# Kernel optimization log

Hardware: AMD Instinct MI355X
Metric: run time of the kernel (lower is better)

## Reference

```python
import jax, jax.numpy as jnp
from jax import lax
import numpy as np

B, C_IN, H, W = 4, 3, 128, 128
K, D = 8192, 16  # num_embeddings, embedding_size (= encoder out channels)


def _conv(x, w, b):
    # x: (B,C,H,W), w: (O,I,3,3) OIHW, VALID padding, stride 1
    y = lax.conv_general_dilated(x, w, (1, 1), 'VALID',
                                 dimension_numbers=('NCHW', 'OIHW', 'NCHW'))
    return y + b[None, :, None, None]


def _conv_t(x, w, b):
    # transpose conv, stride 1, k=3: correlate with flipped/transposed kernel, pad 2
    # w: (I,O,3,3) -> flip spatial, swap to OIHW
    wk = jnp.flip(w, (2, 3)).transpose(1, 0, 2, 3)
    y = lax.conv_general_dilated(x, wk, (1, 1), [(2, 2), (2, 2)],
                                 dimension_numbers=('NCHW', 'OIHW', 'NCHW'))
    return y + b[None, :, None, None]


def setup_inputs() -> dict:
    key = jax.random.key(0)
    ks = jax.random.split(key, 14)
    g = lambda k, shp, fan: jax.random.normal(k, shp, jnp.float32) / np.float32(np.sqrt(fan))
    return {
        'x':   jax.random.normal(ks[0], (B, C_IN, H, W), jnp.float32),
        'ew1': g(ks[1], (4, C_IN, 3, 3), C_IN * 9), 'eb1': jnp.zeros((4,), jnp.float32),
        'ew2': g(ks[2], (8, 4, 3, 3), 4 * 9),       'eb2': jnp.zeros((8,), jnp.float32),
        'ew3': g(ks[3], (16, 8, 3, 3), 8 * 9),      'eb3': jnp.zeros((16,), jnp.float32),
        'dw1': g(ks[4], (16, 8, 3, 3), 16 * 9),     'db1': jnp.zeros((8,), jnp.float32),
        'dw2': g(ks[5], (8, 4, 3, 3), 8 * 9),       'db2': jnp.zeros((4,), jnp.float32),
        'dw3': g(ks[6], (4, C_IN, 3, 3), 4 * 9),    'db3': jnp.zeros((C_IN,), jnp.float32),
        'codebook': jax.random.normal(ks[7], (K, D), jnp.float32) * 0.02,
    }


def reference(x, ew1, eb1, ew2, eb2, ew3, eb3, dw1, db1, dw2, db2, dw3, db3, codebook):
    # encode
    z = jax.nn.selu(_conv(x, ew1, eb1))
    z = jax.nn.selu(_conv(z, ew2, eb2))
    z = _conv(z, ew3, eb3)                      # (B, D, h, w)
    b, d, h, w = z.shape
    zf = z.transpose(0, 2, 3, 1).reshape(-1, d)  # (N, D) flattened latents
    # ||z - e||^2 = ||z||^2 - 2 z.e + ||e||^2, argmin over codebook rows
    d2 = ((zf * zf).sum(1, keepdims=True)
          - 2.0 * (zf @ codebook.T)
          + (codebook * codebook).sum(1)[None, :])  # (N, K)
    idx = jnp.argmin(d2, axis=1)                 # (N,) int32
    zq = codebook[idx].reshape(b, h, w, d).transpose(0, 3, 1, 2)  # gather + reshape
    # decode
    y = jax.nn.selu(_conv_t(zq, dw1, db1))
    y = jax.nn.selu(_conv_t(y, dw2, db2))
    y = _conv_t(y, dw3, db3)                     # (B, C_IN, H, W)
    return (y, idx)
```

## Files before the change

kernel.cpp:

```cpp
#include <hip/hip_runtime.h>
#include <math.h>

#define BATCH 4
#define DLAT 16
#define KCB 8192
#define HLAT 122
#define PIX (HLAT*HLAT)
#define NLAT (BATCH*PIX)
#define NKT (KCB/16)
#define NVQBLK 931
#define KTW (NKT/4)
#define CAPW 1024
#define NCONVBLK 3721

typedef _Float16 half8 __attribute__((ext_vector_type(8)));
typedef float f32x4 __attribute__((ext_vector_type(4)));

__device__ __forceinline__ float selu_np(float x) {
    const float scale = 1.0507009873554805f, alpha = 1.6732632423543772f;
    if (x > 0.f) return __fmul_rn(scale, x);
    return __fmul_rn(scale, __fmul_rn(alpha, expm1f(x)));
}

template<int CI, int CO, int HIN, int WIN, bool DOSELU>
__global__ void conv3x3_np(const float* __restrict__ in, const float* __restrict__ w,
                           const float* __restrict__ bias, float* __restrict__ out) {
    constexpr int HO = HIN - 2, WO = WIN - 2;
    int tid = blockIdx.x * blockDim.x + threadIdx.x;
    constexpr int total = BATCH * CO * HO * WO;
    if (tid >= total) return;
    int j = tid % WO; int t = tid / WO;
    int i = t % HO;   t /= HO;
    int o = t % CO;   int b = t / CO;
    float acc = 0.f;
    for (int c = 0; c < CI; ++c) {
        const float* ip = in + ((b * CI + c) * HIN + i) * WIN + j;
        const float* wp = w + ((o * CI + c) * 3) * 3;
        #pragma unroll
        for (int p = 0; p < 3; ++p)
            #pragma unroll
            for (int q = 0; q < 3; ++q)
                acc = __fmaf_rn(ip[p * WIN + q], wp[p * 3 + q], acc);
    }
    acc = __fadd_rn(acc, bias[o]);
    out[tid] = DOSELU ? selu_np(acc) : acc;
}

__global__ void conv3_last_np(const float* __restrict__ in, const float* __restrict__ w,
                              const float* __restrict__ bias, float* __restrict__ zf,
                              _Float16* __restrict__ zh, float* __restrict__ blockmax) {
    constexpr int CI = 8, HIN = 124, WIN = 124, WO = 122;
    __shared__ float sred[4];
    int tid = blockIdx.x * 256 + threadIdx.x;
    int o  = tid & 15;
    int pp = tid >> 4;
    int b = pp / PIX, pix = pp % PIX;
    int i = pix / WO, j = pix % WO;
    float acc = 0.f;
    for (int c = 0; c < CI; ++c) {
        const float* ip = in + ((b * CI + c) * HIN + i) * WIN + j;
        const float* wp = w + ((o * CI + c) * 3) * 3;
        #pragma unroll
        for (int p = 0; p < 3; ++p)
            #pragma unroll
            for (int q = 0; q < 3; ++q)
                acc = __fmaf_rn(ip[p * WIN + q], wp[p * 3 + q], acc);
    }
    acc = __fadd_rn(acc, bias[o]);
    zf[tid] = acc;
    zh[tid] = (_Float16)acc;
    float m = fabsf(acc);
    #pragma unroll
    for (int off = 32; off; off >>= 1) m = fmaxf(m, __shfl_xor(m, off));
    if ((threadIdx.x & 63) == 0) sred[threadIdx.x >> 6] = m;
    __syncthreads();
    if (threadIdx.x == 0)
        blockmax[blockIdx.x] = fmaxf(fmaxf(sred[0], sred[1]), fmaxf(sred[2], sred[3]));
}

__global__ void reduce_zmax(const float* __restrict__ bm, unsigned* __restrict__ scal) {
    __shared__ float sred[4];
    float m = 0.f;
    for (int i = threadIdx.x; i < NCONVBLK; i += 256) m = fmaxf(m, bm[i]);
    #pragma unroll
    for (int off = 32; off; off >>= 1) m = fmaxf(m, __shfl_xor(m, off));
    if ((threadIdx.x & 63) == 0) sred[threadIdx.x >> 6] = m;
    __syncthreads();
    if (threadIdx.x == 0)
        scal[0] = __float_as_uint(fmaxf(fmaxf(sred[0], sred[1]), fmaxf(sred[2], sred[3])));
}

__device__ __forceinline__ float pairwise16_sq(const float* v) {
    float a[16];
    #pragma unroll
    for (int d = 0; d < 16; ++d) a[d] = __fmul_rn(v[d], v[d]);
    float r0 = __fadd_rn(a[0], a[8]),  r1 = __fadd_rn(a[1], a[9]);
    float r2 = __fadd_rn(a[2], a[10]), r3 = __fadd_rn(a[3], a[11]);
    float r4 = __fadd_rn(a[4], a[12]), r5 = __fadd_rn(a[5], a[13]);
    float r6 = __fadd_rn(a[6], a[14]), r7 = __fadd_rn(a[7], a[15]);
    return __fadd_rn(__fadd_rn(__fadd_rn(r0, r1), __fadd_rn(r2, r3)),
                     __fadd_rn(__fadd_rn(r4, r5), __fadd_rn(r6, r7)));
}

__device__ __forceinline__ void load16(const float* __restrict__ p, float* v) {
    const float4* r = (const float4*)p;
    float4 v0 = r[0], v1 = r[1], v2 = r[2], v3 = r[3];
    v[0]=v0.x; v[1]=v0.y; v[2]=v0.z; v[3]=v0.w;
    v[4]=v1.x; v[5]=v1.y; v[6]=v1.z; v[7]=v1.w;
    v[8]=v2.x; v[9]=v2.y; v[10]=v2.z; v[11]=v2.w;
    v[12]=v3.x; v[13]=v3.y; v[14]=v3.z; v[15]=v3.w;
}

__device__ __forceinline__ float np_d2(const float* zr, float A, const float* e16, float cnk) {
    float g = 0.f;
    #pragma unroll
    for (int d = 0; d < 16; ++d) g = __fmaf_rn(zr[d], e16[d], g);
    return __fadd_rn(__fmaf_rn(-2.f, g, A), cnk);
}

__global__ void init_scal(unsigned* scal) { scal[0] = 0u; scal[1] = 0u; }

__global__ void cbprep(const float* __restrict__ cb, float* __restrict__ cn,
                       _Float16* __restrict__ cbB, unsigned* __restrict__ scal) {
    int k = blockIdx.x * 256 + threadIdx.x;
    float v[16];
    load16(cb + (size_t)k * DLAT, v);
    float C = pairwise16_sq(v);
    cn[k] = C;
    float m = C;
    #pragma unroll
    for (int off = 32; off; off >>= 1) m = fmaxf(m, __shfl_xor(m, off));
    if ((threadIdx.x & 63) == 0) atomicMax(&scal[1], __float_as_uint(m));
    int kt = k >> 4, col = k & 15;
    #pragma unroll
    for (int d = 0; d < 16; ++d) {
        int ln = (d >> 3) * 16 + col;
        cbB[((size_t)(kt * 32 + ln)) * 8 + (d & 7)] = (_Float16)v[d];
    }
}

__global__ __launch_bounds__(256, 4) void vq_mfma(
        const _Float16* __restrict__ zh, const float* __restrict__ zf,
        const _Float16* __restrict__ cbB, const float* __restrict__ cn,
        const float* __restrict__ cb, const unsigned* __restrict__ scal,
        float* __restrict__ idx_out, float* __restrict__ zq) {
    __shared__ unsigned list[CAPW];
    __shared__ float resd[CAPW];
    __shared__ float smin[4][64];
    __shared__ unsigned lcnt;
    const int tid = threadIdx.x;
    const int w = tid >> 6, lane = tid & 63;
    const int R0 = blockIdx.x * 64;
    const half8 hz = {0,0,0,0,0,0,0,0};
    const f32x4 zero4 = {0.f, 0.f, 0.f, 0.f};
    if (tid == 0) lcnt = 0;

    half8 a[4];
    #pragma unroll
    for (int f = 0; f < 4; ++f) {
        int r = R0 + f * 16 + (lane & 15);
        if (r >= NLAT) r = NLAT - 1;
        a[f] = (lane < 32) ? *(const half8*)(zh + (size_t)r * DLAT + (lane >> 4) * 8) : hz;
    }

    float zmaxf = __uint_as_float(scal[0]);
    float en    = sqrtf(__uint_as_float(scal[1]));
    float errG  = 4.f * zmaxf * en * 9.765625e-4f * 1.03f
                + 6.104e-5f * (16.f * zmaxf + 4.f * en);
    float slack = (16.f * zmaxf * zmaxf + 8.f * zmaxf * en + en * en) * 1.2e-7f;
    float DELTA = 4.f * errG + 2.f * slack + 1e-6f;

    const int kt0 = w * KTW, kt1 = kt0 + KTW;

    float m[4][4];
    #pragma unroll
    for (int f = 0; f < 4; ++f)
        #pragma unroll
        for (int j = 0; j < 4; ++j) m[f][j] = INFINITY;

    for (int kt = kt0; kt < kt1; ++kt) {
        half8 b = (lane < 32) ? *(const half8*)(cbB + ((size_t)(kt * 32 + lane)) * 8) : hz;
        float cnv = cn[kt * 16 + (lane & 15)];
        #pragma unroll
        for (int f = 0; f < 4; ++f) {
            f32x4 D = __builtin_amdgcn_mfma_f32_16x16x32_f16(a[f], b, zero4, 0, 0, 0);
            #pragma unroll
            for (int j = 0; j < 4; ++j)
                m[f][j] = fminf(m[f][j], __fmaf_rn(-2.f, D[j], cnv));
        }
    }
    #pragma unroll
    for (int f = 0; f < 4; ++f)
        #pragma unroll
        for (int j = 0; j < 4; ++j) {
            float v = m[f][j];
            v = fminf(v, __shfl_xor(v, 1));
            v = fminf(v, __shfl_xor(v, 2));
            v = fminf(v, __shfl_xor(v, 4));
            v = fminf(v, __shfl_xor(v, 8));
            m[f][j] = v;
        }
    if ((lane & 15) == 0) {
        #pragma unroll
        for (int f = 0; f < 4; ++f)
            #pragma unroll
            for (int j = 0; j < 4; ++j)
                smin[w][f * 16 + (lane >> 4) * 4 + j] = m[f][j];
    }
    __syncthreads();
    #pragma unroll
    for (int f = 0; f < 4; ++f)
        #pragma unroll
        for (int j = 0; j < 4; ++j) {
            int r = f * 16 + (lane >> 4) * 4 + j;
            float v = fminf(fminf(smin[0][r], smin[1][r]), fminf(smin[2][r], smin[3][r]));
            m[f][j] = v + DELTA;
        }

    for (int kt = kt0; kt < kt1; ++kt) {
        half8 b = (lane < 32) ? *(const half8*)(cbB + ((size_t)(kt * 32 + lane)) * 8) : hz;
        float cnv = cn[kt * 16 + (lane & 15)];
        float sv[4][4];
        bool anyp = false;
        #pragma unroll
        for (int f = 0; f < 4; ++f) {
            f32x4 D = __builtin_amdgcn_mfma_f32_16x16x32_f16(a[f], b, zero4, 0, 0, 0);
            #pragma unroll
            for (int j = 0; j < 4; ++j) {
                float s = __fmaf_rn(-2.f, D[j], cnv);
                sv[f][j] = s;
                anyp |= (s <= m[f][j]);
            }
        }
        if (__ballot(anyp)) {
            #pragma unroll
            for (int f = 0; f < 4; ++f)
                #pragma unroll
                for (int j = 0; j < 4; ++j) {
                    bool pred = sv[f][j] <= m[f][j];
                    unsigned long long bal = __ballot(pred);
                    if (bal) {
                        unsigned nb = (unsigned)__popcll(bal);
                        unsigned base = 0;
                        if (lane == 0) base = atomicAdd(&lcnt, nb);
                        base = __shfl(base, 0);
                        unsigned pos = base + (unsigned)__popcll(bal & ((1ull << lane) - 1ull));
                        if (pred && pos < CAPW) {
                            unsigned rs = (unsigned)(f * 16 + (lane >> 4) * 4 + j);
                            list[pos] = (rs << 13) | (unsigned)(kt * 16 + (lane & 15));
                        }
                    }
                }
        }
    }
    __syncthreads();
    unsigned cnt = lcnt;

    if (cnt <= CAPW) {
        for (unsigned i = tid; i < cnt; i += 256) {
            unsigned e = list[i];
            int n = R0 + (int)(e >> 13);
            if (n >= NLAT) n = NLAT - 1;
            int k = (int)(e & 8191);
            float zr[16], e16[16];
            load16(zf + (size_t)n * DLAT, zr);
            float A = pairwise16_sq(zr);
            load16(cb + (size_t)k * DLAT, e16);
            resd[i] = np_d2(zr, A, e16, cn[k]);
        }
    }
    __syncthreads();

    if (tid < 64) {
        int r = R0 + tid;
        if (r < NLAT) {
            float bd = INFINITY; int bk = 0x7fffffff;
            if (cnt <= CAPW) {
                for (unsigned i = 0; i < cnt; ++i) {
                    unsigned e = list[i];
                    if ((int)(e >> 13) == tid) {
                        float d2 = resd[i]; int k = (int)(e & 8191);
                        if (d2 < bd || (d2 == bd && k < bk)) { bd = d2; bk = k; }
                    }
                }
            } else {
                float zr[16];
                load16(zf + (size_t)r * DLAT, zr);
                float A = pairwise16_sq(zr);
                for (int k = 0; k < KCB; ++k) {
                    float e16[16];
                    load16(cb + (size_t)k * DLAT, e16);
                    float d2 = np_d2(zr, A, e16, cn[k]);
                    if (d2 < bd) { bd = d2; bk = k; }
                }
            }
            idx_out[r] = (float)bk;
            int b = r / PIX, pix = r % PIX;
            const float* e = cb + (size_t)bk * DLAT;
            #pragma unroll
            for (int d = 0; d < DLAT; ++d) zq[((size_t)(b * DLAT + d)) * PIX + pix] = e[d];
        }
    }
}

template<int CI, int CO, int HIN, int WIN, bool DOSELU>
__global__ void convt3x3(const float* __restrict__ in, const float* __restrict__ w,
                         const float* __restrict__ bias, float* __restrict__ out) {
    constexpr int HO = HIN + 2, WO = WIN + 2;
    int tid = blockIdx.x * blockDim.x + threadIdx.x;
    constexpr int total = BATCH * CO * HO * WO;
    if (tid >= total) return;
    int j = tid % WO; int t = tid / WO;
    int i = t % HO;   t /= HO;
    int o = t % CO;   int b = t / CO;
    float acc = bias[o];
    for (int c = 0; c < CI; ++c) {
        const float* ip = in + ((b * CI + c) * HIN) * WIN;
        const float* wp = w + ((c * CO + o) * 3) * 3;
        #pragma unroll
        for (int p = 0; p < 3; ++p) {
            int ii = i + p - 2;
            if (ii < 0 || ii >= HIN) continue;
            #pragma unroll
            for (int q = 0; q < 3; ++q) {
                int jj = j + q - 2;
                if (jj < 0 || jj >= WIN) continue;
                acc += ip[ii * WIN + jj] * wp[(2 - p) * 3 + (2 - q)];
            }
        }
    }
    const float scale = 1.0507009873554805f, alpha = 1.6732632423543772f;
    out[tid] = DOSELU ? (acc > 0.f ? scale * acc : scale * alpha * (expf(acc) - 1.f)) : acc;
}

extern "C" void kernel_launch(void* const* d_in, const int* in_sizes, int n_in,
                              void* d_out, int out_size, void* d_ws, size_t ws_size,
                              hipStream_t stream) {
    const float* x   = (const float*)d_in[0];
    const float* ew1 = (const float*)d_in[1];  const float* eb1 = (const float*)d_in[2];
    const float* ew2 = (const float*)d_in[3];  const float* eb2 = (const float*)d_in[4];
    const float* ew3 = (const float*)d_in[5];  const float* eb3 = (const float*)d_in[6];
    const float* dw1 = (const float*)d_in[7];  const float* db1 = (const float*)d_in[8];
    const float* dw2 = (const float*)d_in[9];  const float* db2 = (const float*)d_in[10];
    const float* dw3 = (const float*)d_in[11]; const float* db3 = (const float*)d_in[12];
    const float* cb  = (const float*)d_in[13];

    float* out_y   = (float*)d_out;
    float* out_idx = (float*)d_out + 196608;

    float*     ws   = (float*)d_ws;
    float*     zf   = ws;
    float*     e1   = ws + 952576;
    float*     e2   = ws + 1206592;
    float*     fZq  = ws + 952576;
    float*     fB   = ws + 1905152;
    float*     fA   = ws + 2397184;
    _Float16*  zh   = (_Float16*)(ws + 2651200);
    _Float16*  cbB  = (_Float16*)(ws + 3127488);
    float*     cn   = ws + 3193024;
    unsigned*  scal = (unsigned*)(ws + 3201216);
    float*     bmax = ws + 3201218;

    const int TPB = 256;

    init_scal<<<1, 1, 0, stream>>>(scal);

    conv3x3_np<3, 4, 128, 128, true ><<<993,  TPB, 0, stream>>>(x,  ew1, eb1, e1);
    conv3x3_np<4, 8, 126, 126, true ><<<1922, TPB, 0, stream>>>(e1, ew2, eb2, e2);
    conv3_last_np<<<NCONVBLK, TPB, 0, stream>>>(e2, ew3, eb3, zf, zh, bmax);
    reduce_zmax<<<1, TPB, 0, stream>>>(bmax, scal);

    cbprep<<<32, TPB, 0, stream>>>(cb, cn, cbB, scal);
    vq_mfma<<<NVQBLK, TPB, 0, stream>>>(zh, zf, cbB, cn, cb, scal, out_idx, fZq);

    convt3x3<16, 8, 122, 122, true ><<<1922, TPB, 0, stream>>>(fZq, dw1, db1, fB);
    convt3x3<8, 4, 124, 124, true ><<<993,  TPB, 0, stream>>>(fB,  dw2, db2, fA);
    convt3x3<4, 3, 126, 126, false><<<768,  TPB, 0, stream>>>(fA,  dw3, db3, out_y);
}
```

Baseline: 262.1 us.

## Fold codebook norm and -2 scale into MFMA via augmented K lanes

The latent is pre-scaled by -2 in fp16, and the codebook tile gains an extra K slot holding the fp16 squared norm, with matching 1.0 entries in the A operand. The MFMA therefore yields -2 z·e + ||e||² directly, removing the per-element fma and the cn load from both scan loops, and the loop is unrolled by 2. The separate init kernel is dropped by resetting scal[1] inside reduce_zmax. The error bound DELTA is widened to cover fp16 rounding of the norm, which may admit more candidates for fp32 re-check.

```diff
diff --git a/kernel.cpp b/kernel.cpp
--- a/kernel.cpp
+++ b/kernel.cpp
@@ -7,9 +7,11 @@
 #define HLAT 122
 #define PIX (HLAT*HLAT)
 #define NLAT (BATCH*PIX)
-#define NKT (KCB/16)
+#define NT16 (KCB/16)
+#define ROWSB 64
 #define NVQBLK 931
-#define KTW (NKT/4)
+#define NWAVE 4
+#define TW (NT16/NWAVE)
 #define CAPW 1024
 #define NCONVBLK 3721
 
@@ -48,7 +50,7 @@
 
 __global__ void conv3_last_np(const float* __restrict__ in, const float* __restrict__ w,
                               const float* __restrict__ bias, float* __restrict__ zf,
-                              _Float16* __restrict__ zh, float* __restrict__ blockmax) {
+                              _Float16* __restrict__ zh2, float* __restrict__ blockmax) {
     constexpr int CI = 8, HIN = 124, WIN = 124, WO = 122;
     __shared__ float sred[4];
     int tid = blockIdx.x * 256 + threadIdx.x;
@@ -68,7 +70,7 @@
     }
     acc = __fadd_rn(acc, bias[o]);
     zf[tid] = acc;
-    zh[tid] = (_Float16)acc;
+    zh2[tid] = (_Float16)(__fmul_rn(-2.f, acc));
     float m = fabsf(acc);
     #pragma unroll
     for (int off = 32; off; off >>= 1) m = fmaxf(m, __shfl_xor(m, off));
@@ -88,6 +90,7 @@
     __syncthreads();
     if (threadIdx.x == 0)
         scal[0] = __float_as_uint(fmaxf(fmaxf(sred[0], sred[1]), fmaxf(sred[2], sred[3])));
+    if (threadIdx.x == 1) scal[1] = 0u;
 }
 
 __device__ __forceinline__ float pairwise16_sq(const float* v) {
@@ -117,8 +120,6 @@
     for (int d = 0; d < 16; ++d) g = __fmaf_rn(zr[d], e16[d], g);
     return __fadd_rn(__fmaf_rn(-2.f, g, A), cnk);
 }
-
-__global__ void init_scal(unsigned* scal) { scal[0] = 0u; scal[1] = 0u; }
 
 __global__ void cbprep(const float* __restrict__ cb, float* __restrict__ cn,
                        _Float16* __restrict__ cbB, unsigned* __restrict__ scal) {
@@ -131,95 +132,112 @@
     #pragma unroll
     for (int off = 32; off; off >>= 1) m = fmaxf(m, __shfl_xor(m, off));
     if ((threadIdx.x & 63) == 0) atomicMax(&scal[1], __float_as_uint(m));
-    int kt = k >> 4, col = k & 15;
-    #pragma unroll
-    for (int d = 0; d < 16; ++d) {
-        int ln = (d >> 3) * 16 + col;
-        cbB[((size_t)(kt * 32 + ln)) * 8 + (d & 7)] = (_Float16)v[d];
-    }
+    int tile = k >> 4, col = k & 15;
+    _Float16* base = cbB + (size_t)tile * 512;
+    #pragma unroll
+    for (int d = 0; d < 16; ++d)
+        base[((d >> 3) * 16 + col) * 8 + (d & 7)] = (_Float16)v[d];
+    base[(32 + col) * 8 + 0] = (_Float16)C;
+    #pragma unroll
+    for (int i = 1; i < 8; ++i) base[(32 + col) * 8 + i] = (_Float16)0.f;
+    #pragma unroll
+    for (int i = 0; i < 8; ++i) base[(48 + col) * 8 + i] = (_Float16)0.f;
 }
 
 __global__ __launch_bounds__(256, 4) void vq_mfma(
-        const _Float16* __restrict__ zh, const float* __restrict__ zf,
+        const _Float16* __restrict__ zh2, const float* __restrict__ zf,
         const _Float16* __restrict__ cbB, const float* __restrict__ cn,
         const float* __restrict__ cb, const unsigned* __restrict__ scal,
         float* __restrict__ idx_out, float* __restrict__ zq) {
     __shared__ unsigned list[CAPW];
     __shared__ float resd[CAPW];
-    __shared__ float smin[4][64];
+    __shared__ float smin[NWAVE][ROWSB];
     __shared__ unsigned lcnt;
     const int tid = threadIdx.x;
     const int w = tid >> 6, lane = tid & 63;
-    const int R0 = blockIdx.x * 64;
-    const half8 hz = {0,0,0,0,0,0,0,0};
+    const int g = lane >> 4;
+    const int col = lane & 15;
+    const int R0 = blockIdx.x * ROWSB;
     const f32x4 zero4 = {0.f, 0.f, 0.f, 0.f};
     if (tid == 0) lcnt = 0;
 
     half8 a[4];
-    #pragma unroll
-    for (int f = 0; f < 4; ++f) {
-        int r = R0 + f * 16 + (lane & 15);
-        if (r >= NLAT) r = NLAT - 1;
-        a[f] = (lane < 32) ? *(const half8*)(zh + (size_t)r * DLAT + (lane >> 4) * 8) : hz;
+    if (lane < 32) {
+        #pragma unroll
+        for (int f = 0; f < 4; ++f) {
+            int r = R0 + f * 16 + col;
+            if (r >= NLAT) r = NLAT - 1;
+            a[f] = *(const half8*)(zh2 + (size_t)r * DLAT + (lane >> 4) * 8);
+        }
+    } else {
+        half8 c = {0,0,0,0,0,0,0,0};
+        if (lane < 48) c[0] = (_Float16)1.f;
+        #pragma unroll
+        for (int f = 0; f < 4; ++f) a[f] = c;
     }
 
     float zmaxf = __uint_as_float(scal[0]);
     float en    = sqrtf(__uint_as_float(scal[1]));
-    float errG  = 4.f * zmaxf * en * 9.765625e-4f * 1.03f
-                + 6.104e-5f * (16.f * zmaxf + 4.f * en);
+    float errG  = 8.f * zmaxf * en * 9.765625e-4f * 1.03f
+                + 6.104e-5f * (32.f * zmaxf + 4.f * en)
+                + 4.882813e-4f * en * en;
     float slack = (16.f * zmaxf * zmaxf + 8.f * zmaxf * en + en * en) * 1.2e-7f;
     float DELTA = 4.f * errG + 2.f * slack + 1e-6f;
 
-    const int kt0 = w * KTW, kt1 = kt0 + KTW;
-
-    float m[4][4];
+    const int t0 = w * TW, t1 = t0 + TW;
+
+    float mm[4][4];
     #pragma unroll
     for (int f = 0; f < 4; ++f)
         #pragma unroll
-        for (int j = 0; j < 4; ++j) m[f][j] = INFINITY;
-
-    for (int kt = kt0; kt < kt1; ++kt) {
-        half8 b = (lane < 32) ? *(const half8*)(cbB + ((size_t)(kt * 32 + lane)) * 8) : hz;
-        float cnv = cn[kt * 16 + (lane & 15)];
+        for (int j = 0; j < 4; ++j) mm[f][j] = INFINITY;
+
+    const _Float16* bptr = cbB + (size_t)t0 * 512 + lane * 8;
+    #pragma unroll 2
+    for (int t = t0; t < t1; ++t) {
+        half8 b = *(const half8*)bptr;
         #pragma unroll
         for (int f = 0; f < 4; ++f) {
             f32x4 D = __builtin_amdgcn_mfma_f32_16x16x32_f16(a[f], b, zero4, 0, 0, 0);
             #pragma unroll
-            for (int j = 0; j < 4; ++j)
-                m[f][j] = fminf(m[f][j], __fmaf_rn(-2.f, D[j], cnv));
-        }
+            for (int j = 0; j < 4; ++j) mm[f][j] = fminf(mm[f][j], D[j]);
+        }
+        bptr += 512;
     }
     #pragma unroll
     for (int f = 0; f < 4; ++f)
         #pragma unroll
         for (int j = 0; j < 4; ++j) {
-            float v = m[f][j];
+            float v = mm[f][j];
             v = fminf(v, __shfl_xor(v, 1));
             v = fminf(v, __shfl_xor(v, 2));
             v = fminf(v, __shfl_xor(v, 4));
             v = fminf(v, __shfl_xor(v, 8));
-            m[f][j] = v;
-        }
-    if ((lane & 15) == 0) {
+            mm[f][j] = v;
+        }
+    if (col == 0) {
         #pragma unroll
         for (int f = 0; f < 4; ++f)
             #pragma unroll
             for (int j = 0; j < 4; ++j)
-                smin[w][f * 16 + (lane >> 4) * 4 + j] = m[f][j];
+                smin[w][f * 16 + g * 4 + j] = mm[f][j];
     }
     __syncthreads();
     #pragma unroll
     for (int f = 0; f < 4; ++f)
         #pragma unroll
         for (int j = 0; j < 4; ++j) {
-            int r = f * 16 + (lane >> 4) * 4 + j;
-            float v = fminf(fminf(smin[0][r], smin[1][r]), fminf(smin[2][r], smin[3][r]));
-            m[f][j] = v + DELTA;
-        }
-
-    for (int kt = kt0; kt < kt1; ++kt) {
-        half8 b = (lane < 32) ? *(const half8*)(cbB + ((size_t)(kt * 32 + lane)) * 8) : hz;
-        float cnv = cn[kt * 16 + (lane & 15)];
+            int row = f * 16 + g * 4 + j;
+            float v = INFINITY;
+            #pragma unroll
+            for (int ww = 0; ww < NWAVE; ++ww) v = fminf(v, smin[ww][row]);
+            mm[f][j] = v + DELTA;
+        }
+
+    bptr = cbB + (size_t)t0 * 512 + lane * 8;
+    #pragma unroll 2
+    for (int t = t0; t < t1; ++t) {
+        half8 b = *(const half8*)bptr;
         float sv[4][4];
         bool anyp = false;
         #pragma unroll
@@ -227,9 +245,8 @@
             f32x4 D = __builtin_amdgcn_mfma_f32_16x16x32_f16(a[f], b, zero4, 0, 0, 0);
             #pragma unroll
             for (int j = 0; j < 4; ++j) {
-                float s = __fmaf_rn(-2.f, D[j], cnv);
-                sv[f][j] = s;
-                anyp |= (s <= m[f][j]);
+                sv[f][j] = D[j];
+                anyp |= (D[j] <= mm[f][j]);
             }
         }
         if (__ballot(anyp)) {
@@ -237,7 +254,7 @@
             for (int f = 0; f < 4; ++f)
                 #pragma unroll
                 for (int j = 0; j < 4; ++j) {
-                    bool pred = sv[f][j] <= m[f][j];
+                    bool pred = sv[f][j] <= mm[f][j];
                     unsigned long long bal = __ballot(pred);
                     if (bal) {
                         unsigned nb = (unsigned)__popcll(bal);
@@ -246,12 +263,13 @@
                         base = __shfl(base, 0);
                         unsigned pos = base + (unsigned)__popcll(bal & ((1ull << lane) - 1ull));
                         if (pred && pos < CAPW) {
-                            unsigned rs = (unsigned)(f * 16 + (lane >> 4) * 4 + j);
-                            list[pos] = (rs << 13) | (unsigned)(kt * 16 + (lane & 15));
+                            unsigned rs = (unsigned)(f * 16 + g * 4 + j);
+                            list[pos] = (rs << 13) | (unsigned)(t * 16 + col);
                         }
                     }
                 }
         }
+        bptr += 512;
     }
     __syncthreads();
     unsigned cnt = lcnt;
@@ -271,7 +289,7 @@
     }
     __syncthreads();
 
-    if (tid < 64) {
+    if (tid < ROWSB) {
         int r = R0 + tid;
         if (r < NLAT) {
             float bd = INFINITY; int bk = 0x7fffffff;
@@ -355,23 +373,21 @@
     float*     fZq  = ws + 952576;
     float*     fB   = ws + 1905152;
     float*     fA   = ws + 2397184;
-    _Float16*  zh   = (_Float16*)(ws + 2651200);
+    _Float16*  zh2  = (_Float16*)(ws + 2651200);
     _Float16*  cbB  = (_Float16*)(ws + 3127488);
-    float*     cn   = ws + 3193024;
-    unsigned*  scal = (unsigned*)(ws + 3201216);
-    float*     bmax = ws + 3201218;
+    float*     cn   = ws + 3258560;
+    unsigned*  scal = (unsigned*)(ws + 3266752);
+    float*     bmax = ws + 3266754;
 
     const int TPB = 256;
-
-    init_scal<<<1, 1, 0, stream>>>(scal);
 
     conv3x3_np<3, 4, 128, 128, true ><<<993,  TPB, 0, stream>>>(x,  ew1, eb1, e1);
     conv3x3_np<4, 8, 126, 126, true ><<<1922, TPB, 0, stream>>>(e1, ew2, eb2, e2);
-    conv3_last_np<<<NCONVBLK, TPB, 0, stream>>>(e2, ew3, eb3, zf, zh, bmax);
+    conv3_last_np<<<NCONVBLK, TPB, 0, stream>>>(e2, ew3, eb3, zf, zh2, bmax);
     reduce_zmax<<<1, TPB, 0, stream>>>(bmax, scal);
 
     cbprep<<<32, TPB, 0, stream>>>(cb, cn, cbB, scal);
-    vq_mfma<<<NVQBLK, TPB, 0, stream>>>(zh, zf, cbB, cn, cb, scal, out_idx, fZq);
+    vq_mfma<<<NVQBLK, TPB, 0, stream>>>(zh2, zf, cbB, cn, cb, scal, out_idx, fZq);
 
     convt3x3<16, 8, 122, 122, true ><<<1922, TPB, 0, stream>>>(fZq, dw1, db1, fB);
     convt3x3<8, 4, 124, 124, true ><<<993,  TPB, 0, stream>>>(fB,  dw2, db2, fA);
```

After: 299.9 us. +14.4%, slower.
